# Optimization experiments

Hardware: AMD Instinct MI355X
Metric: run time of the kernel (lower is better)

Reference implementation:

```python
import jax, jax.numpy as jnp
import numpy as np
from jax import lax

NPOINT = 1024
RADIUS = 0.2
NSAMPLE = 32
BN_EPS = 1e-5


def square_distance(src, dst):
    # src: [B,N,3], dst: [B,M,3] -> [B,N,M]
    d = -2.0 * jnp.einsum('bnc,bmc->bnm', src, dst)
    d = d + jnp.sum(src * src, -1)[:, :, None]
    d = d + jnp.sum(dst * dst, -1)[:, None, :]
    return d


def farthest_point_sample(xyz, npoint):
    # Deterministic start at index 0 (torch version uses a random start).
    B, N, _ = xyz.shape
    batch = jnp.arange(B)

    def step(carry, _):
        distance, farthest = carry
        centroid = xyz[batch, farthest][:, None, :]          # [B,1,3]
        dist = jnp.sum((xyz - centroid) ** 2, -1)            # [B,N]
        distance = jnp.minimum(distance, dist)
        new_far = jnp.argmax(distance, -1).astype(jnp.int32)
        return (distance, new_far), farthest

    init = (jnp.full((B, N), 1e10, xyz.dtype), jnp.zeros((B,), jnp.int32))
    _, cents = lax.scan(step, init, None, length=npoint)     # [npoint,B]
    return cents.T                                           # [B,npoint]


def index_points(points, idx):
    # points: [B,N,C], idx: [B,...] -> [B,...,C]
    return jax.vmap(lambda p, i: p[i])(points, idx)


def query_ball_point(radius, nsample, xyz, new_xyz):
    B, N, _ = xyz.shape
    sqr = square_distance(new_xyz, xyz)                      # [B,S,N]
    gidx = jnp.where(sqr > radius * radius, N,
                     jnp.arange(N, dtype=jnp.int32)[None, None, :])
    gidx = jnp.sort(gidx, axis=-1)[:, :, :nsample]           # [B,S,nsample]
    first = gidx[:, :, :1]
    return jnp.where(gidx == N, first, gidx)


def conv_bn_relu(x, w, b, g, beta):
    # x: [B,Cin,K,S]; 1x1 conv + training-mode BN + ReLU
    y = jnp.einsum('bcks,oc->boks', x, w) + b[None, :, None, None]
    mean = jnp.mean(y, axis=(0, 2, 3), keepdims=True)
    var = jnp.var(y, axis=(0, 2, 3), keepdims=True)
    y = (y - mean) * lax.rsqrt(var + BN_EPS)
    y = y * g[None, :, None, None] + beta[None, :, None, None]
    return jax.nn.relu(y)


def setup_inputs() -> dict:
    key = jax.random.key(0)
    ks = jax.random.split(key, 8)
    B, N, D = 16, 4096, 64
    inp = {
        'xyz': jax.random.uniform(ks[0], (B, N, 3), jnp.float32),
        'points': jax.random.normal(ks[1], (B, N, D), jnp.float32),
        'w1': jax.random.normal(ks[2], (64, 67), jnp.float32) * 0.1,
        'b1': jax.random.normal(ks[3], (64,), jnp.float32) * 0.1,
        'g1': jnp.ones((64,), jnp.float32),
        'beta1': jnp.zeros((64,), jnp.float32),
        'w2': jax.random.normal(ks[4], (64, 64), jnp.float32) * 0.1,
        'b2': jax.random.normal(ks[5], (64,), jnp.float32) * 0.1,
        'g2': jnp.ones((64,), jnp.float32),
        'beta2': jnp.zeros((64,), jnp.float32),
        'w3': jax.random.normal(ks[6], (128, 64), jnp.float32) * 0.1,
        'b3': jax.random.normal(ks[7], (128,), jnp.float32) * 0.1,
        'g3': jnp.ones((128,), jnp.float32),
        'beta3': jnp.zeros((128,), jnp.float32),
    }
    return inp


def reference(xyz, points, w1, b1, g1, beta1, w2, b2, g2, beta2, w3, b3, g3, beta3):
    B, N, C = xyz.shape
    fps_idx = farthest_point_sample(xyz, NPOINT)                 # [B,S]
    new_xyz = index_points(xyz, fps_idx)                         # [B,S,3]
    idx = query_ball_point(RADIUS, NSAMPLE, xyz, new_xyz)        # [B,S,K]
    grouped_xyz = index_points(xyz, idx) - new_xyz[:, :, None, :]  # [B,S,K,3]
    grouped_points = jnp.concatenate([grouped_xyz, index_points(points, idx)], axis=-1)  # [B,S,K,3+D]
    x = jnp.transpose(grouped_points, (0, 3, 2, 1))              # [B,C,K,S]
    x = conv_bn_relu(x, w1, b1, g1, beta1)
    x = conv_bn_relu(x, w2, b2, g2, beta2)
    x = conv_bn_relu(x, w3, b3, g3, beta3)
    new_points = jnp.max(x, axis=2)                              # [B,C_out,S]
    new_points = jnp.transpose(new_points, (0, 2, 1))            # [B,S,C_out]
    return (new_xyz, new_points)
```

## Files before the change

### kernel.cpp

```cpp
#include <hip/hip_runtime.h>
#include <stdint.h>

#define NPOINT 1024
#define NSAMPLE 32
#define NB 16
#define NN 4096
#define BN_EPS 1e-5
#define NPIX (NB*NPOINT*NSAMPLE)
#define NBLK 8192

__device__ __forceinline__ float sqdist3(float dx, float dy, float dz) {
  #pragma clang fp contract(off)
  float a = dx*dx; float b = dy*dy; float c = dz*dz;
  return (a + b) + c;
}

#define FPS_T 256
#define FPS_PTS (NN/FPS_T)
#define FPS_W (FPS_T/64)

#define DPP_MAX64V(VAR, CTRL)                                                  \
  {                                                                            \
    long long kl = __double_as_longlong(VAR);                                  \
    int lo = (int)(unsigned int)kl, hi = (int)(kl >> 32);                      \
    int olo = __builtin_amdgcn_update_dpp(lo, lo, (CTRL), 0xf, 0xf, false);    \
    int ohi = __builtin_amdgcn_update_dpp(hi, hi, (CTRL), 0xf, 0xf, false);    \
    double ok = __longlong_as_double(((long long)ohi << 32) |                  \
                                     (unsigned long long)(unsigned int)olo);   \
    VAR = fmax(VAR, ok);                                                       \
  }

__global__ __launch_bounds__(256) void fps_kernel(
    const float* __restrict__ xyz, int* __restrict__ cents_g,
    float* __restrict__ out_xyz) {
  __shared__ __align__(16) float4 pos[NN];
  __shared__ __align__(16) double keybuf[2][FPS_W];
  __shared__ int cents_l[NPOINT];
  const int b = blockIdx.x;
  const int t = threadIdx.x;
  const float* base = xyz + (size_t)b * NN * 3;
  for (int i = t; i < NN; i += FPS_T) {
    pos[i] = make_float4(base[3*i+0], base[3*i+1], base[3*i+2], 0.f);
  }
  __syncthreads();
  float px[FPS_PTS], py[FPS_PTS], pz[FPS_PTS], dist[FPS_PTS];
  int lowj[FPS_PTS];
  #pragma unroll
  for (int i = 0; i < FPS_PTS; i++) {
    float4 p = pos[i*FPS_T + t];
    px[i] = p.x; py[i] = p.y; pz[i] = p.z;
    dist[i] = 1e10f;
    lowj[i] = (NN-1) - (i*FPS_T + t);
  }
  const int lane = t & 63, wid = t >> 6;
  int far = 0;
  for (int it = 0; it < NPOINT; it++) {
    if (t == 0) cents_l[it] = far;
    float4 c = pos[far];
    float nd[FPS_PTS];
    #pragma unroll
    for (int i = 0; i < FPS_PTS; i++) {
      float d = sqdist3(px[i]-c.x, py[i]-c.y, pz[i]-c.z);
      nd[i] = fminf(dist[i], d);
      dist[i] = nd[i];
    }
    double kk[FPS_PTS];
    #pragma unroll
    for (int i = 0; i < FPS_PTS; i++) {
      kk[i] = __longlong_as_double(
          ((long long)__float_as_int(nd[i]) << 32) |
          (unsigned long long)(unsigned int)lowj[i]);
    }
    double m0 = fmax(fmax(kk[0],  kk[1]),  fmax(kk[2],  kk[3]));
    double m1 = fmax(fmax(kk[4],  kk[5]),  fmax(kk[6],  kk[7]));
    double m2 = fmax(fmax(kk[8],  kk[9]),  fmax(kk[10], kk[11]));
    double m3 = fmax(fmax(kk[12], kk[13]), fmax(kk[14], kk[15]));
    double bk = fmax(fmax(m0, m1), fmax(m2, m3));
    DPP_MAX64V(bk, 0x111);
    DPP_MAX64V(bk, 0x112);
    DPP_MAX64V(bk, 0x114);
    DPP_MAX64V(bk, 0x118);
    DPP_MAX64V(bk, 0x142);
    DPP_MAX64V(bk, 0x143);
    const int p = it & 1;
    if (lane == 63) keybuf[p][wid] = bk;
    __syncthreads();
    double k = keybuf[p][lane & (FPS_W-1)];
    DPP_MAX64V(k, 0x111);
    DPP_MAX64V(k, 0x112);
    int lo32 = (int)(unsigned int)__double_as_longlong(k);
    far = (NN-1) - __builtin_amdgcn_readlane(lo32, 3);
  }
  __syncthreads();
  for (int i = t; i < NPOINT; i += FPS_T) {
    int j = cents_l[i];
    cents_g[b*NPOINT + i] = j;
    float4 p = pos[j];
    size_t o = ((size_t)b * NPOINT + i) * 3;
    out_xyz[o+0] = p.x;
    out_xyz[o+1] = p.y;
    out_xyz[o+2] = p.z;
  }
}

__global__ __launch_bounds__(256) void ballquery_kernel(
    const float* __restrict__ xyz, const int* __restrict__ cents_g,
    int* __restrict__ idx) {
  const int w = blockIdx.x * 4 + (threadIdx.x >> 6);
  const int lane = threadIdx.x & 63;
  const int b = w >> 10;
  const double RR = 0.2 * 0.2;
  const int cj = cents_g[w] & (NN-1);
  const float* cptr = xyz + ((size_t)b * NN + cj) * 3;
  const double cx = (double)cptr[0], cy = (double)cptr[1], cz = (double)cptr[2];
  const double cn = cx*cx + cy*cy + cz*cz;
  const float* base = xyz + (size_t)b * NN * 3;
  int* out = idx + (size_t)w * NSAMPLE;
  int have = 0, firstj = 0;
  for (int j0 = 0; j0 < NN; j0 += 64) {
    int j = j0 + lane;
    double x = (double)base[3*j+0];
    double y = (double)base[3*j+1];
    double z = (double)base[3*j+2];
    double pn = x*x + y*y + z*z;
    double d = -2.0*(cx*x + cy*y + cz*z) + cn + pn;
    bool pass = !(d > RR);
    unsigned long long m = __ballot(pass);
    int cnt = __popcll(m);
    if (have == 0 && cnt > 0) firstj = j0 + (__ffsll((unsigned long long)m) - 1);
    if (pass) {
      int pos = have + __popcll(m & ((1ull << lane) - 1ull));
      if (pos < NSAMPLE) out[pos] = j;
    }
    have += cnt;
    if (have >= NSAMPLE) break;
  }
  for (int k = have + lane; k < NSAMPLE; k += 64) out[k] = firstj;
}

template<int MODE, bool STOREY>
__global__ __launch_bounds__(256) void fused_pass(
    const float* __restrict__ xyz, const float* __restrict__ points,
    const int* __restrict__ cents_g, const int* __restrict__ idx,
    const float* __restrict__ w1, const float* __restrict__ b1,
    const float* __restrict__ w2, const float* __restrict__ b2,
    const float* __restrict__ w3, const float* __restrict__ b3,
    const double* __restrict__ aff1, const double* __restrict__ aff2,
    double* __restrict__ partial, float* __restrict__ pmax, float* __restrict__ pmin,
    float* __restrict__ ystore) {
  __shared__ float wbuf[67*64];
  __shared__ float xsm[67*68];
  __shared__ float bsm[64];
  __shared__ float bsm2[64];
  __shared__ float sc1m[64], sh1m[64], sc2m[64], sh2m[64];
  const int t = threadIdx.x;
  const int pb = blockIdx.x * 64;
  const int tr = t & 15, tc = t >> 4;
  double* pout = partial + (size_t)blockIdx.x * 256;

  for (int ii = t; ii < 67*64; ii += 256) {
    int oc = ii & 63, cc = ii >> 6;
    wbuf[cc*64 + oc] = w1[oc*67 + cc];
  }
  if (t < 64) {
    bsm[t] = b1[t];
    if (MODE >= 2) { sc1m[t] = (float)aff1[t]; sh1m[t] = (float)aff1[128+t]; }
    if (MODE >= 3) { sc2m[t] = (float)aff2[t]; sh2m[t] = (float)aff2[128+t]; }
  }
  {
    const int pxl = t >> 2, q = t & 3;
    const int p = pb + pxl;
    const int bs = p >> 5;
    const int b  = p >> 15;
    const int j  = idx[p] & (NN-1);
    const float4* prow = (const float4*)(points + ((size_t)b * NN + j) * 64);
    #pragma unroll
    for (int u = 0; u < 4; u++) {
      float4 v = prow[q*4 + u];
      int c0 = 3 + q*16 + u*4;
      xsm[(c0+0)*68 + pxl] = v.x;
      xsm[(c0+1)*68 + pxl] = v.y;
      xsm[(c0+2)*68 + pxl] = v.z;
      xsm[(c0+3)*68 + pxl] = v.w;
    }
    if (q == 0) {
      const float* xr = xyz + ((size_t)b * NN + j) * 3;
      const int cj = cents_g[bs] & (NN-1);
      const float* ce = xyz + ((size_t)b * NN + cj) * 3;
      xsm[0*68 + pxl] = xr[0] - ce[0];
      xsm[1*68 + pxl] = xr[1] - ce[1];
      xsm[2*68 + pxl] = xr[2] - ce[2];
    }
  }
  __syncthreads();

  float acc[4][4] = {};
  for (int cc = 0; cc < 67; cc++) {
    float4 xv = *(const float4*)&xsm[cc*68 + 4*tr];
    float4 wv = *(const float4*)&wbuf[cc*64 + 4*tc];
    float xa[4] = {xv.x, xv.y, xv.z, xv.w};
    float wa[4] = {wv.x, wv.y, wv.z, wv.w};
    #pragma unroll
    for (int i = 0; i < 4; i++)
      #pragma unroll
      for (int jj = 0; jj < 4; jj++) acc[i][jj] += xa[i]*wa[jj];
  }
  if constexpr (MODE == 1) {
    if constexpr (STOREY) {
      #pragma unroll
      for (int i = 0; i < 4; i++) {
        float4 o = make_float4(acc[i][0], acc[i][1], acc[i][2], acc[i][3]);
        *(float4*)(ystore + ((size_t)(pb + 4*tr + i))*64 + 4*tc) = o;
      }
    }
    double s1[4] = {0,0,0,0}, s2[4] = {0,0,0,0};
    #pragma unroll
    for (int jj = 0; jj < 4; jj++) {
      float bb = bsm[4*tc+jj];
      #pragma unroll
      for (int i = 0; i < 4; i++) {
        double yd = (double)(acc[i][jj] + bb);
        s1[jj] += yd; s2[jj] += yd*yd;
      }
    }
    #pragma unroll
    for (int off = 8; off > 0; off >>= 1)
      #pragma unroll
      for (int jj = 0; jj < 4; jj++) {
        s1[jj] += __shfl_down(s1[jj], off, 16);
        s2[jj] += __shfl_down(s2[jj], off, 16);
      }
    if (tr == 0)
      #pragma unroll
      for (int jj = 0; jj < 4; jj++) {
        pout[4*tc+jj]       = s1[jj];
        pout[128 + 4*tc+jj] = s2[jj];
      }
    return;
  }

  __syncthreads();
  #pragma unroll
  for (int jj = 0; jj < 4; jj++) {
    int oc = 4*tc + jj;
    float bb = bsm[oc], sc = sc1m[oc], sh = sh1m[oc];
    float r[4];
    #pragma unroll
    for (int i = 0; i < 4; i++) r[i] = fmaxf((acc[i][jj] + bb)*sc + sh, 0.f);
    *(float4*)&xsm[oc*68 + 4*tr] = make_float4(r[0], r[1], r[2], r[3]);
  }
  for (int ii = t; ii < 4096; ii += 256) {
    int oc = ii & 63, cc = ii >> 6;
    wbuf[cc*64 + oc] = w2[oc*64 + cc];
  }
  if (t < 64) bsm2[t] = b2[t];
  __syncthreads();

  float acc2[4][4] = {};
  for (int cc = 0; cc < 64; cc++) {
    float4 xv = *(const float4*)&xsm[cc*68 + 4*tr];
    float4 wv = *(const float4*)&wbuf[cc*64 + 4*tc];
    float xa[4] = {xv.x, xv.y, xv.z, xv.w};
    float wa[4] = {wv.x, wv.y, wv.z, wv.w};
    #pragma unroll
    for (int i = 0; i < 4; i++)
      #pragma unroll
      for (int jj = 0; jj < 4; jj++) acc2[i][jj] += xa[i]*wa[jj];
  }
  if constexpr (MODE == 2) {
    if constexpr (STOREY) {
      #pragma unroll
      for (int i = 0; i < 4; i++) {
        float4 o = make_float4(acc2[i][0], acc2[i][1], acc2[i][2], acc2[i][3]);
        *(float4*)(ystore + ((size_t)(pb + 4*tr + i))*64 + 4*tc) = o;
      }
    }
    double s1[4] = {0,0,0,0}, s2[4] = {0,0,0,0};
    #pragma unroll
    for (int jj = 0; jj < 4; jj++) {
      float bb = bsm2[4*tc+jj];
      #pragma unroll
      for (int i = 0; i < 4; i++) {
        double yd = (double)(acc2[i][jj] + bb);
        s1[jj] += yd; s2[jj] += yd*yd;
      }
    }
    #pragma unroll
    for (int off = 8; off > 0; off >>= 1)
      #pragma unroll
      for (int jj = 0; jj < 4; jj++) {
        s1[jj] += __shfl_down(s1[jj], off, 16);
        s2[jj] += __shfl_down(s2[jj], off, 16);
      }
    if (tr == 0)
      #pragma unroll
      for (int jj = 0; jj < 4; jj++) {
        pout[4*tc+jj]       = s1[jj];
        pout[128 + 4*tc+jj] = s2[jj];
      }
    return;
  }

  if constexpr (MODE == 3) {
    __syncthreads();
    #pragma unroll
    for (int jj = 0; jj < 4; jj++) {
      int oc = 4*tc + jj;
      float bb = bsm2[oc], sc = sc2m[oc], sh = sh2m[oc];
      float r[4];
      #pragma unroll
      for (int i = 0; i < 4; i++) r[i] = fmaxf((acc2[i][jj] + bb)*sc + sh, 0.f);
      *(float4*)&xsm[oc*68 + 4*tr] = make_float4(r[0], r[1], r[2], r[3]);
    }
    for (int h = 0; h < 2; h++) {
      for (int ii = t; ii < 4096; ii += 256) {
        int oc = ii & 63, cc = ii >> 6;
        wbuf[cc*64 + oc] = w3[(h*64 + oc)*64 + cc];
      }
      if (t < 64) bsm[t] = b3[h*64 + t];
      __syncthreads();
      float acc3[4][4] = {};
      for (int cc = 0; cc < 64; cc++) {
        float4 xv = *(const float4*)&xsm[cc*68 + 4*tr];
        float4 wv = *(const float4*)&wbuf[cc*64 + 4*tc];
        float xa[4] = {xv.x, xv.y, xv.z, xv.w};
        float wa[4] = {wv.x, wv.y, wv.z, wv.w};
        #pragma unroll
        for (int i = 0; i < 4; i++)
          #pragma unroll
          for (int jj = 0; jj < 4; jj++) acc3[i][jj] += xa[i]*wa[jj];
      }
      double s1[4] = {0,0,0,0}, s2[4] = {0,0,0,0};
      float pmx[4], pmn[4];
      #pragma unroll
      for (int jj = 0; jj < 4; jj++) { pmx[jj] = -3.4e38f; pmn[jj] = 3.4e38f; }
      #pragma unroll
      for (int jj = 0; jj < 4; jj++) {
        float bb = bsm[4*tc+jj];
        #pragma unroll
        for (int i = 0; i < 4; i++) {
          float y = acc3[i][jj] + bb;
          double yd = (double)y;
          s1[jj] += yd; s2[jj] += yd*yd;
          pmx[jj] = fmaxf(pmx[jj], y); pmn[jj] = fminf(pmn[jj], y);
        }
      }
      #pragma unroll
      for (int off = 8; off > 0; off >>= 1)
        #pragma unroll
        for (int jj = 0; jj < 4; jj++) {
          s1[jj] += __shfl_down(s1[jj], off, 16);
          s2[jj] += __shfl_down(s2[jj], off, 16);
        }
      if (tr == 0)
        #pragma unroll
        for (int jj = 0; jj < 4; jj++) {
          pout[h*64 + 4*tc+jj]       = s1[jj];
          pout[128 + h*64 + 4*tc+jj] = s2[jj];
        }
      #pragma unroll
      for (int off = 4; off > 0; off >>= 1)
        #pragma unroll
        for (int jj = 0; jj < 4; jj++) {
          pmx[jj] = fmaxf(pmx[jj], __shfl_down(pmx[jj], off, 8));
          pmn[jj] = fminf(pmn[jj], __shfl_down(pmn[jj], off, 8));
        }
      if ((tr & 7) == 0) {
        int bs = (pb >> 5) + (tr >> 3);
        size_t ob = (size_t)bs*128 + h*64 + 4*tc;
        #pragma unroll
        for (int jj = 0; jj < 4; jj++) {
          pmax[ob + jj] = pmx[jj];
          pmin[ob + jj] = pmn[jj];
        }
      }
      __syncthreads();
    }
  }
}

__global__ __launch_bounds__(256) void fused_mid(
    const float* __restrict__ y1, const float* __restrict__ b1,
    const float* __restrict__ w2, const float* __restrict__ b2,
    const double* __restrict__ aff1,
    double* __restrict__ partial, float* __restrict__ y2) {
  __shared__ float wbuf[64*64];
  __shared__ float xsm[64*68];
  __shared__ float bsm[64];
  __shared__ float bsm2[64];
  __shared__ float sc1m[64], sh1m[64];
  const int t = threadIdx.x;
  const int pb = blockIdx.x * 64;
  const int tr = t & 15, tc = t >> 4;
  double* pout = partial + (size_t)blockIdx.x * 256;

  for (int ii = t; ii < 4096; ii += 256) {
    int oc = ii & 63, cc = ii >> 6;
    wbuf[cc*64 + oc] = w2[oc*64 + cc];
  }
  if (t < 64) {
    bsm[t] = b1[t]; bsm2[t] = b2[t];
    sc1m[t] = (float)aff1[t]; sh1m[t] = (float)aff1[128+t];
  }
  __syncthreads();
  {
    const int pxl = t >> 2, q = t & 3;
    const float* yrow = y1 + ((size_t)(pb + pxl))*64;
    #pragma unroll
    for (int u = 0; u < 4; u++) {
      int c0 = 4*q + 16*u;
      float4 v = *(const float4*)(yrow + c0);
      xsm[(c0+0)*68 + pxl] = fmaxf((v.x + bsm[c0+0])*sc1m[c0+0] + sh1m[c0+0], 0.f);
      xsm[(c0+1)*68 + pxl] = fmaxf((v.y + bsm[c0+1])*sc1m[c0+1] + sh1m[c0+1], 0.f);
      xsm[(c0+2)*68 + pxl] = fmaxf((v.z + bsm[c0+2])*sc1m[c0+2] + sh1m[c0+2], 0.f);
      xsm[(c0+3)*68 + pxl] = fmaxf((v.w + bsm[c0+3])*sc1m[c0+3] + sh1m[c0+3], 0.f);
    }
  }
  __syncthreads();

  float acc2[4][4] = {};
  for (int cc = 0; cc < 64; cc++) {
    float4 xv = *(const float4*)&xsm[cc*68 + 4*tr];
    float4 wv = *(const float4*)&wbuf[cc*64 + 4*tc];
    float xa[4] = {xv.x, xv.y, xv.z, xv.w};
    float wa[4] = {wv.x, wv.y, wv.z, wv.w};
    #pragma unroll
    for (int i = 0; i < 4; i++)
      #pragma unroll
      for (int jj = 0; jj < 4; jj++) acc2[i][jj] += xa[i]*wa[jj];
  }
  #pragma unroll
  for (int i = 0; i < 4; i++) {
    float4 o = make_float4(acc2[i][0], acc2[i][1], acc2[i][2], acc2[i][3]);
    *(float4*)(y2 + ((size_t)(pb + 4*tr + i))*64 + 4*tc) = o;
  }
  double s1[4] = {0,0,0,0}, s2[4] = {0,0,0,0};
  #pragma unroll
  for (int jj = 0; jj < 4; jj++) {
    float bb = bsm2[4*tc+jj];
    #pragma unroll
    for (int i = 0; i < 4; i++) {
      double yd = (double)(acc2[i][jj] + bb);
      s1[jj] += yd; s2[jj] += yd*yd;
    }
  }
  #pragma unroll
  for (int off = 8; off > 0; off >>= 1)
    #pragma unroll
    for (int jj = 0; jj < 4; jj++) {
      s1[jj] += __shfl_down(s1[jj], off, 16);
      s2[jj] += __shfl_down(s2[jj], off, 16);
    }
  if (tr == 0)
    #pragma unroll
    for (int jj = 0; jj < 4; jj++) {
      pout[4*tc+jj]       = s1[jj];
      pout[128 + 4*tc+jj] = s2[jj];
    }
}

__global__ __launch_bounds__(256) void fused_last(
    const float* __restrict__ y2, const float* __restrict__ b2,
    const float* __restrict__ w3, const float* __restrict__ b3,
    const double* __restrict__ aff2,
    double* __restrict__ partial, float* __restrict__ pmax, float* __restrict__ pmin) {
  __shared__ float wbuf[64*64];
  __shared__ float xsm[64*68];
  __shared__ float bsm[64];
  __shared__ float bsm2[64];
  __shared__ float sc2m[64], sh2m[64];
  const int t = threadIdx.x;
  const int pb = blockIdx.x * 64;
  const int tr = t & 15, tc = t >> 4;
  double* pout = partial + (size_t)blockIdx.x * 256;

  if (t < 64) {
    bsm2[t] = b2[t];
    sc2m[t] = (float)aff2[t]; sh2m[t] = (float)aff2[128+t];
  }
  __syncthreads();
  {
    const int pxl = t >> 2, q = t & 3;
    const float* yrow = y2 + ((size_t)(pb + pxl))*64;
    #pragma unroll
    for (int u = 0; u < 4; u++) {
      int c0 = 4*q + 16*u;
      float4 v = *(const float4*)(yrow + c0);
      xsm[(c0+0)*68 + pxl] = fmaxf((v.x + bsm2[c0+0])*sc2m[c0+0] + sh2m[c0+0], 0.f);
      xsm[(c0+1)*68 + pxl] = fmaxf((v.y + bsm2[c0+1])*sc2m[c0+1] + sh2m[c0+1], 0.f);
      xsm[(c0+2)*68 + pxl] = fmaxf((v.z + bsm2[c0+2])*sc2m[c0+2] + sh2m[c0+2], 0.f);
      xsm[(c0+3)*68 + pxl] = fmaxf((v.w + bsm2[c0+3])*sc2m[c0+3] + sh2m[c0+3], 0.f);
    }
  }
  for (int h = 0; h < 2; h++) {
    for (int ii = t; ii < 4096; ii += 256) {
      int oc = ii & 63, cc = ii >> 6;
      wbuf[cc*64 + oc] = w3[(h*64 + oc)*64 + cc];
    }
    if (t < 64) bsm[t] = b3[h*64 + t];
    __syncthreads();
    float acc3[4][4] = {};
    for (int cc = 0; cc < 64; cc++) {
      float4 xv = *(const float4*)&xsm[cc*68 + 4*tr];
      float4 wv = *(const float4*)&wbuf[cc*64 + 4*tc];
      float xa[4] = {xv.x, xv.y, xv.z, xv.w};
      float wa[4] = {wv.x, wv.y, wv.z, wv.w};
      #pragma unroll
      for (int i = 0; i < 4; i++)
        #pragma unroll
        for (int jj = 0; jj < 4; jj++) acc3[i][jj] += xa[i]*wa[jj];
    }
    double s1[4] = {0,0,0,0}, s2[4] = {0,0,0,0};
    float pmx[4], pmn[4];
    #pragma unroll
    for (int jj = 0; jj < 4; jj++) { pmx[jj] = -3.4e38f; pmn[jj] = 3.4e38f; }
    #pragma unroll
    for (int jj = 0; jj < 4; jj++) {
      float bb = bsm[4*tc+jj];
      #pragma unroll
      for (int i = 0; i < 4; i++) {
        float y = acc3[i][jj] + bb;
        double yd = (double)y;
        s1[jj] += yd; s2[jj] += yd*yd;
        pmx[jj] = fmaxf(pmx[jj], y); pmn[jj] = fminf(pmn[jj], y);
      }
    }
    #pragma unroll
    for (int off = 8; off > 0; off >>= 1)
      #pragma unroll
      for (int jj = 0; jj < 4; jj++) {
        s1[jj] += __shfl_down(s1[jj], off, 16);
        s2[jj] += __shfl_down(s2[jj], off, 16);
      }
    if (tr == 0)
      #pragma unroll
      for (int jj = 0; jj < 4; jj++) {
        pout[h*64 + 4*tc+jj]       = s1[jj];
        pout[128 + h*64 + 4*tc+jj] = s2[jj];
      }
    #pragma unroll
    for (int off = 4; off > 0; off >>= 1)
      #pragma unroll
      for (int jj = 0; jj < 4; jj++) {
        pmx[jj] = fmaxf(pmx[jj], __shfl_down(pmx[jj], off, 8));
        pmn[jj] = fminf(pmn[jj], __shfl_down(pmn[jj], off, 8));
      }
    if ((tr & 7) == 0) {
      int bs = (pb >> 5) + (tr >> 3);
      size_t ob = (size_t)bs*128 + h*64 + 4*tc;
      #pragma unroll
      for (int jj = 0; jj < 4; jj++) {
        pmax[ob + jj] = pmx[jj];
        pmin[ob + jj] = pmn[jj];
      }
    }
    __syncthreads();
  }
}

__global__ __launch_bounds__(256) void reduce_stageA(
    const double* __restrict__ partial, double* __restrict__ partial2) {
  const int t = threadIdx.x;
  const int bid = blockIdx.x;
  const double* p = partial + (size_t)bid * 64 * 256 + t;
  double a0 = 0.0, a1 = 0.0, a2 = 0.0, a3 = 0.0;
  #pragma unroll 4
  for (int i = 0; i < 64; i += 4) {
    a0 += p[(size_t)(i+0)*256];
    a1 += p[(size_t)(i+1)*256];
    a2 += p[(size_t)(i+2)*256];
    a3 += p[(size_t)(i+3)*256];
  }
  partial2[(size_t)bid*256 + t] = (a0 + a1) + (a2 + a3);
}

__global__ __launch_bounds__(256) void reduce_finalize_kernel(
    const double* __restrict__ partial2,
    const float* __restrict__ g, const float* __restrict__ beta,
    double* __restrict__ aff) {
  __shared__ double sa1[4], sa2[4];
  const int c = blockIdx.x;
  const int t = threadIdx.x;
  double a1 = 0.0, a2 = 0.0;
  for (int blk = t; blk < 128; blk += 256) {
    a1 += partial2[(size_t)blk*256 + c];
    a2 += partial2[(size_t)blk*256 + 128 + c];
  }
  #pragma unroll
  for (int off = 32; off > 0; off >>= 1) {
    a1 += __shfl_down(a1, off);
    a2 += __shfl_down(a2, off);
  }
  const int lane = t & 63, wid = t >> 6;
  if (lane == 0) { sa1[wid] = a1; sa2[wid] = a2; }
  __syncthreads();
  if (t == 0) {
    double s1 = sa1[0] + sa1[1] + sa1[2] + sa1[3];
    double s2 = sa2[0] + sa2[1] + sa2[2] + sa2[3];
    const double invN = 1.0 / (double)NPIX;
    double mean = s1 * invN;
    double var  = s2 * invN - mean*mean;
    var = var > 0.0 ? var : 0.0;
    double r  = 1.0 / sqrt(var + BN_EPS);
    double sc = (double)g[c] * r;
    aff[c]       = sc;
    aff[128 + c] = (double)beta[c] - mean*sc;
  }
}

__global__ __launch_bounds__(256) void out_kernel(
    const float* __restrict__ pmax, const float* __restrict__ pmin,
    const double* __restrict__ aff3, float* __restrict__ out_np) {
  int i = blockIdx.x * 256 + threadIdx.x;
  int oc = i & 127;
  double sc = aff3[oc], sh = aff3[128+oc];
  double v = (sc >= 0.0) ? (double)pmax[i] : (double)pmin[i];
  double y = v*sc + sh;
  out_np[i] = (float)(y > 0.0 ? y : 0.0);
}

extern "C" void kernel_launch(void* const* d_in, const int* in_sizes, int n_in,
                              void* d_out, int out_size, void* d_ws, size_t ws_size,
                              hipStream_t stream) {
  const float* xyz    = (const float*)d_in[0];
  const float* points = (const float*)d_in[1];
  const float* w1  = (const float*)d_in[2];
  const float* b1  = (const float*)d_in[3];
  const float* g1  = (const float*)d_in[4];
  const float* be1 = (const float*)d_in[5];
  const float* w2  = (const float*)d_in[6];
  const float* b2  = (const float*)d_in[7];
  const float* g2  = (const float*)d_in[8];
  const float* be2 = (const float*)d_in[9];
  const float* w3  = (const float*)d_in[10];
  const float* b3  = (const float*)d_in[11];
  const float* g3  = (const float*)d_in[12];
  const float* be3 = (const float*)d_in[13];

  char* ws = (char*)d_ws;
  double* aff     = (double*)(ws + 8192);
  int*    cents   = (int*)  (ws + 16384);
  int*    idx     = (int*)  (ws + 81920);
  float*  pmax    = (float*)(ws + 2179072);
  float*  pmin    = (float*)(ws + 10567680);
  double* partial = (double*)(ws + 18956288);
  const size_t OFF_Y = 35733504;
  const size_t SZ_Y  = (size_t)NPIX * 64 * 4;
  float* ycache1 = (float*)(ws + OFF_Y);
  float* ycache2 = (float*)(ws + OFF_Y + SZ_Y);
  const bool full_path = ws_size >= OFF_Y + 2*SZ_Y;
  const bool mid_path  = ws_size >= OFF_Y + SZ_Y;
  double* p2a = (double*)pmax;
  double* p2b = (double*)idx;
  float* out_xyz = (float*)d_out;
  float* out_np  = (float*)d_out + (size_t)NB*NPOINT*3;

  fps_kernel        <<<16,   256, 0, stream>>>(xyz, cents, out_xyz);
  ballquery_kernel  <<<4096, 256, 0, stream>>>(xyz, cents, idx);
  if (full_path) {
    fused_pass<1,true>  <<<NBLK, 256, 0, stream>>>(xyz, points, cents, idx, w1,b1,w2,b2,w3,b3,
                                                   aff, aff+256, partial, pmax, pmin, ycache1);
    reduce_stageA     <<<128, 256, 0, stream>>>(partial, p2a);
    reduce_finalize_kernel<<<64, 256, 0, stream>>>(p2a, g1, be1, aff);
    fused_mid         <<<NBLK, 256, 0, stream>>>(ycache1, b1, w2, b2, aff, partial, ycache2);
    reduce_stageA     <<<128, 256, 0, stream>>>(partial, p2a);
    reduce_finalize_kernel<<<64, 256, 0, stream>>>(p2a, g2, be2, aff+256);
    fused_last        <<<NBLK, 256, 0, stream>>>(ycache2, b2, w3, b3, aff+256,
                                                 partial, pmax, pmin);
    reduce_stageA     <<<128, 256, 0, stream>>>(partial, p2b);
    reduce_finalize_kernel<<<128, 256, 0, stream>>>(p2b, g3, be3, aff+512);
  } else if (mid_path) {
    fused_pass<1,false> <<<NBLK, 256, 0, stream>>>(xyz, points, cents, idx, w1,b1,w2,b2,w3,b3,
                                                   aff, aff+256, partial, pmax, pmin, nullptr);
    reduce_stageA     <<<128, 256, 0, stream>>>(partial, p2a);
    reduce_finalize_kernel<<<64, 256, 0, stream>>>(p2a, g1, be1, aff);
    fused_pass<2,true>  <<<NBLK, 256, 0, stream>>>(xyz, points, cents, idx, w1,b1,w2,b2,w3,b3,
                                                   aff, aff+256, partial, pmax, pmin, ycache1);
    reduce_stageA     <<<128, 256, 0, stream>>>(partial, p2a);
    reduce_finalize_kernel<<<64, 256, 0, stream>>>(p2a, g2, be2, aff+256);
    fused_last        <<<NBLK, 256, 0, stream>>>(ycache1, b2, w3, b3, aff+256,
                                                 partial, pmax, pmin);
    reduce_stageA     <<<128, 256, 0, stream>>>(partial, p2b);
    reduce_finalize_kernel<<<128, 256, 0, stream>>>(p2b, g3, be3, aff+512);
  } else {
    fused_pass<1,false> <<<NBLK, 256, 0, stream>>>(xyz, points, cents, idx, w1,b1,w2,b2,w3,b3,
                                                   aff, aff+256, partial, pmax, pmin, nullptr);
    reduce_stageA     <<<128, 256, 0, stream>>>(partial, p2a);
    reduce_finalize_kernel<<<64, 256, 0, stream>>>(p2a, g1, be1, aff);
    fused_pass<2,false> <<<NBLK, 256, 0, stream>>>(xyz, points, cents, idx, w1,b1,w2,b2,w3,b3,
                                                   aff, aff+256, partial, pmax, pmin, nullptr);
    reduce_stageA     <<<128, 256, 0, stream>>>(partial, p2a);
    reduce_finalize_kernel<<<64, 256, 0, stream>>>(p2a, g2, be2, aff+256);
    fused_pass<3,false> <<<NBLK, 256, 0, stream>>>(xyz, points, cents, idx, w1,b1,w2,b2,w3,b3,
                                                   aff, aff+256, partial, pmax, pmin, nullptr);
    reduce_stageA     <<<128, 256, 0, stream>>>(partial, p2b);
    reduce_finalize_kernel<<<128, 256, 0, stream>>>(p2b, g3, be3, aff+512);
  }
  out_kernel        <<<NBLK, 256, 0, stream>>>(pmax, pmin, aff+512, out_np);
}
```

Before: 1.194 ms.

## Process two pixel tiles per block in layers 1-2 and pack FPS distance keys

Adds dedicated first-layer and mid-layer kernels that each handle two 64-pixel tiles per block, halving the block count. This amortizes the per-block weight transpose into shared memory and halves the per-block BN partial sums, so the reduction kernels get a block-count parameter. FPS now keeps packed distance/index keys in doubles and updates them with a single fmin, which removes the separate float distance array and the repack step. Fewer blocks may reduce occupancy and latency hiding.

```diff
diff --git a/kernel.cpp b/kernel.cpp
--- a/kernel.cpp
+++ b/kernel.cpp
@@ -8,6 +8,7 @@
 #define BN_EPS 1e-5
 #define NPIX (NB*NPOINT*NSAMPLE)
 #define NBLK 8192
+#define NBLK2 4096
 
 __device__ __forceinline__ float sqdist3(float dx, float dy, float dz) {
   #pragma clang fp contract(off)
@@ -43,33 +44,30 @@
     pos[i] = make_float4(base[3*i+0], base[3*i+1], base[3*i+2], 0.f);
   }
   __syncthreads();
-  float px[FPS_PTS], py[FPS_PTS], pz[FPS_PTS], dist[FPS_PTS];
+  float px[FPS_PTS], py[FPS_PTS], pz[FPS_PTS];
+  double kk[FPS_PTS];
   int lowj[FPS_PTS];
   #pragma unroll
   for (int i = 0; i < FPS_PTS; i++) {
     float4 p = pos[i*FPS_T + t];
     px[i] = p.x; py[i] = p.y; pz[i] = p.z;
-    dist[i] = 1e10f;
     lowj[i] = (NN-1) - (i*FPS_T + t);
+    kk[i] = __longlong_as_double(
+        ((long long)__float_as_int(1e10f) << 32) |
+        (unsigned long long)(unsigned int)lowj[i]);
   }
   const int lane = t & 63, wid = t >> 6;
   int far = 0;
   for (int it = 0; it < NPOINT; it++) {
     if (t == 0) cents_l[it] = far;
     float4 c = pos[far];
-    float nd[FPS_PTS];
     #pragma unroll
     for (int i = 0; i < FPS_PTS; i++) {
       float d = sqdist3(px[i]-c.x, py[i]-c.y, pz[i]-c.z);
-      nd[i] = fminf(dist[i], d);
-      dist[i] = nd[i];
-    }
-    double kk[FPS_PTS];
-    #pragma unroll
-    for (int i = 0; i < FPS_PTS; i++) {
-      kk[i] = __longlong_as_double(
-          ((long long)__float_as_int(nd[i]) << 32) |
+      double nk = __longlong_as_double(
+          ((long long)__float_as_int(d) << 32) |
           (unsigned long long)(unsigned int)lowj[i]);
+      kk[i] = fmin(kk[i], nk);
     }
     double m0 = fmax(fmax(kk[0],  kk[1]),  fmax(kk[2],  kk[3]));
     double m1 = fmax(fmax(kk[4],  kk[5]),  fmax(kk[6],  kk[7]));
@@ -138,6 +136,281 @@
   for (int k = have + lane; k < NSAMPLE; k += 64) out[k] = firstj;
 }
 
+__global__ __launch_bounds__(256) void fused_first2(
+    const float* __restrict__ xyz, const float* __restrict__ points,
+    const int* __restrict__ cents_g, const int* __restrict__ idx,
+    const float* __restrict__ w1, const float* __restrict__ b1,
+    double* __restrict__ partial, float* __restrict__ ystore) {
+  __shared__ float wbuf[67*64];
+  __shared__ float xsm[67*68];
+  __shared__ float bsm[64];
+  const int t = threadIdx.x;
+  const int pb0 = blockIdx.x * 128;
+  const int tr = t & 15, tc = t >> 4;
+  double* pout = partial + (size_t)blockIdx.x * 256;
+
+  for (int ii = t; ii < 67*64; ii += 256) {
+    int oc = ii & 63, cc = ii >> 6;
+    wbuf[cc*64 + oc] = w1[oc*67 + cc];
+  }
+  if (t < 64) bsm[t] = b1[t];
+
+  double s1[4] = {0,0,0,0}, s2[4] = {0,0,0,0};
+  for (int tile = 0; tile < 2; tile++) {
+    const int pb = pb0 + tile*64;
+    if (tile) __syncthreads();
+    {
+      const int pxl = t >> 2, q = t & 3;
+      const int p = pb + pxl;
+      const int bs = p >> 5;
+      const int b  = p >> 15;
+      const int j  = idx[p] & (NN-1);
+      const float4* prow = (const float4*)(points + ((size_t)b * NN + j) * 64);
+      #pragma unroll
+      for (int u = 0; u < 4; u++) {
+        float4 v = prow[q*4 + u];
+        int c0 = 3 + q*16 + u*4;
+        xsm[(c0+0)*68 + pxl] = v.x;
+        xsm[(c0+1)*68 + pxl] = v.y;
+        xsm[(c0+2)*68 + pxl] = v.z;
+        xsm[(c0+3)*68 + pxl] = v.w;
+      }
+      if (q == 0) {
+        const float* xr = xyz + ((size_t)b * NN + j) * 3;
+        const int cj = cents_g[bs] & (NN-1);
+        const float* ce = xyz + ((size_t)b * NN + cj) * 3;
+        xsm[0*68 + pxl] = xr[0] - ce[0];
+        xsm[1*68 + pxl] = xr[1] - ce[1];
+        xsm[2*68 + pxl] = xr[2] - ce[2];
+      }
+    }
+    __syncthreads();
+
+    float acc[4][4] = {};
+    for (int cc = 0; cc < 67; cc++) {
+      float4 xv = *(const float4*)&xsm[cc*68 + 4*tr];
+      float4 wv = *(const float4*)&wbuf[cc*64 + 4*tc];
+      float xa[4] = {xv.x, xv.y, xv.z, xv.w};
+      float wa[4] = {wv.x, wv.y, wv.z, wv.w};
+      #pragma unroll
+      for (int i = 0; i < 4; i++)
+        #pragma unroll
+        for (int jj = 0; jj < 4; jj++) acc[i][jj] += xa[i]*wa[jj];
+    }
+    #pragma unroll
+    for (int i = 0; i < 4; i++) {
+      float4 o = make_float4(acc[i][0], acc[i][1], acc[i][2], acc[i][3]);
+      *(float4*)(ystore + ((size_t)(pb + 4*tr + i))*64 + 4*tc) = o;
+    }
+    #pragma unroll
+    for (int jj = 0; jj < 4; jj++) {
+      float bb = bsm[4*tc+jj];
+      #pragma unroll
+      for (int i = 0; i < 4; i++) {
+        double yd = (double)(acc[i][jj] + bb);
+        s1[jj] += yd; s2[jj] += yd*yd;
+      }
+    }
+  }
+  #pragma unroll
+  for (int off = 8; off > 0; off >>= 1)
+    #pragma unroll
+    for (int jj = 0; jj < 4; jj++) {
+      s1[jj] += __shfl_down(s1[jj], off, 16);
+      s2[jj] += __shfl_down(s2[jj], off, 16);
+    }
+  if (tr == 0)
+    #pragma unroll
+    for (int jj = 0; jj < 4; jj++) {
+      pout[4*tc+jj]       = s1[jj];
+      pout[128 + 4*tc+jj] = s2[jj];
+    }
+}
+
+__global__ __launch_bounds__(256) void fused_mid2(
+    const float* __restrict__ y1, const float* __restrict__ b1,
+    const float* __restrict__ w2, const float* __restrict__ b2,
+    const double* __restrict__ aff1,
+    double* __restrict__ partial, float* __restrict__ y2) {
+  __shared__ float wbuf[64*64];
+  __shared__ float xsm[64*68];
+  __shared__ float bsm[64];
+  __shared__ float bsm2[64];
+  __shared__ float sc1m[64], sh1m[64];
+  const int t = threadIdx.x;
+  const int pb0 = blockIdx.x * 128;
+  const int tr = t & 15, tc = t >> 4;
+  double* pout = partial + (size_t)blockIdx.x * 256;
+
+  for (int ii = t; ii < 4096; ii += 256) {
+    int oc = ii & 63, cc = ii >> 6;
+    wbuf[cc*64 + oc] = w2[oc*64 + cc];
+  }
+  if (t < 64) {
+    bsm[t] = b1[t]; bsm2[t] = b2[t];
+    sc1m[t] = (float)aff1[t]; sh1m[t] = (float)aff1[128+t];
+  }
+
+  double s1[4] = {0,0,0,0}, s2[4] = {0,0,0,0};
+  for (int tile = 0; tile < 2; tile++) {
+    const int pb = pb0 + tile*64;
+    if (tile) __syncthreads();
+    else __syncthreads();
+    {
+      const int pxl = t >> 2, q = t & 3;
+      const float* yrow = y1 + ((size_t)(pb + pxl))*64;
+      #pragma unroll
+      for (int u = 0; u < 4; u++) {
+        int c0 = 4*q + 16*u;
+        float4 v = *(const float4*)(yrow + c0);
+        xsm[(c0+0)*68 + pxl] = fmaxf((v.x + bsm[c0+0])*sc1m[c0+0] + sh1m[c0+0], 0.f);
+        xsm[(c0+1)*68 + pxl] = fmaxf((v.y + bsm[c0+1])*sc1m[c0+1] + sh1m[c0+1], 0.f);
+        xsm[(c0+2)*68 + pxl] = fmaxf((v.z + bsm[c0+2])*sc1m[c0+2] + sh1m[c0+2], 0.f);
+        xsm[(c0+3)*68 + pxl] = fmaxf((v.w + bsm[c0+3])*sc1m[c0+3] + sh1m[c0+3], 0.f);
+      }
+    }
+    __syncthreads();
+
+    float acc2[4][4] = {};
+    for (int cc = 0; cc < 64; cc++) {
+      float4 xv = *(const float4*)&xsm[cc*68 + 4*tr];
+      float4 wv = *(const float4*)&wbuf[cc*64 + 4*tc];
+      float xa[4] = {xv.x, xv.y, xv.z, xv.w};
+      float wa[4] = {wv.x, wv.y, wv.z, wv.w};
+      #pragma unroll
+      for (int i = 0; i < 4; i++)
+        #pragma unroll
+        for (int jj = 0; jj < 4; jj++) acc2[i][jj] += xa[i]*wa[jj];
+    }
+    #pragma unroll
+    for (int i = 0; i < 4; i++) {
+      float4 o = make_float4(acc2[i][0], acc2[i][1], acc2[i][2], acc2[i][3]);
+      *(float4*)(y2 + ((size_t)(pb + 4*tr + i))*64 + 4*tc) = o;
+    }
+    #pragma unroll
+    for (int jj = 0; jj < 4; jj++) {
+      float bb = bsm2[4*tc+jj];
+      #pragma unroll
+      for (int i = 0; i < 4; i++) {
+        double yd = (double)(acc2[i][jj] + bb);
+        s1[jj] += yd; s2[jj] += yd*yd;
+      }
+    }
+  }
+  #pragma unroll
+  for (int off = 8; off > 0; off >>= 1)
+    #pragma unroll
+    for (int jj = 0; jj < 4; jj++) {
+      s1[jj] += __shfl_down(s1[jj], off, 16);
+      s2[jj] += __shfl_down(s2[jj], off, 16);
+    }
+  if (tr == 0)
+    #pragma unroll
+    for (int jj = 0; jj < 4; jj++) {
+      pout[4*tc+jj]       = s1[jj];
+      pout[128 + 4*tc+jj] = s2[jj];
+    }
+}
+
+__global__ __launch_bounds__(256) void fused_last(
+    const float* __restrict__ y2, const float* __restrict__ b2,
+    const float* __restrict__ w3, const float* __restrict__ b3,
+    const double* __restrict__ aff2,
+    double* __restrict__ partial, float* __restrict__ pmax, float* __restrict__ pmin) {
+  __shared__ float wbuf[64*64];
+  __shared__ float xsm[64*68];
+  __shared__ float bsm[64];
+  __shared__ float bsm2[64];
+  __shared__ float sc2m[64], sh2m[64];
+  const int t = threadIdx.x;
+  const int pb = blockIdx.x * 64;
+  const int tr = t & 15, tc = t >> 4;
+  double* pout = partial + (size_t)blockIdx.x * 256;
+
+  if (t < 64) {
+    bsm2[t] = b2[t];
+    sc2m[t] = (float)aff2[t]; sh2m[t] = (float)aff2[128+t];
+  }
+  __syncthreads();
+  {
+    const int pxl = t >> 2, q = t & 3;
+    const float* yrow = y2 + ((size_t)(pb + pxl))*64;
+    #pragma unroll
+    for (int u = 0; u < 4; u++) {
+      int c0 = 4*q + 16*u;
+      float4 v = *(const float4*)(yrow + c0);
+      xsm[(c0+0)*68 + pxl] = fmaxf((v.x + bsm2[c0+0])*sc2m[c0+0] + sh2m[c0+0], 0.f);
+      xsm[(c0+1)*68 + pxl] = fmaxf((v.y + bsm2[c0+1])*sc2m[c0+1] + sh2m[c0+1], 0.f);
+      xsm[(c0+2)*68 + pxl] = fmaxf((v.z + bsm2[c0+2])*sc2m[c0+2] + sh2m[c0+2], 0.f);
+      xsm[(c0+3)*68 + pxl] = fmaxf((v.w + bsm2[c0+3])*sc2m[c0+3] + sh2m[c0+3], 0.f);
+    }
+  }
+  for (int h = 0; h < 2; h++) {
+    for (int ii = t; ii < 4096; ii += 256) {
+      int oc = ii & 63, cc = ii >> 6;
+      wbuf[cc*64 + oc] = w3[(h*64 + oc)*64 + cc];
+    }
+    if (t < 64) bsm[t] = b3[h*64 + t];
+    __syncthreads();
+    float acc3[4][4] = {};
+    for (int cc = 0; cc < 64; cc++) {
+      float4 xv = *(const float4*)&xsm[cc*68 + 4*tr];
+      float4 wv = *(const float4*)&wbuf[cc*64 + 4*tc];
+      float xa[4] = {xv.x, xv.y, xv.z, xv.w};
+      float wa[4] = {wv.x, wv.y, wv.z, wv.w};
+      #pragma unroll
+      for (int i = 0; i < 4; i++)
+        #pragma unroll
+        for (int jj = 0; jj < 4; jj++) acc3[i][jj] += xa[i]*wa[jj];
+    }
+    double s1[4] = {0,0,0,0}, s2[4] = {0,0,0,0};
+    float pmx[4], pmn[4];
+    #pragma unroll
+    for (int jj = 0; jj < 4; jj++) { pmx[jj] = -3.4e38f; pmn[jj] = 3.4e38f; }
+    #pragma unroll
+    for (int jj = 0; jj < 4; jj++) {
+      float bb = bsm[4*tc+jj];
+      #pragma unroll
+      for (int i = 0; i < 4; i++) {
+        float y = acc3[i][jj] + bb;
+        double yd = (double)y;
+        s1[jj] += yd; s2[jj] += yd*yd;
+        pmx[jj] = fmaxf(pmx[jj], y); pmn[jj] = fminf(pmn[jj], y);
+      }
+    }
+    #pragma unroll
+    for (int off = 8; off > 0; off >>= 1)
+      #pragma unroll
+      for (int jj = 0; jj < 4; jj++) {
+        s1[jj] += __shfl_down(s1[jj], off, 16);
+        s2[jj] += __shfl_down(s2[jj], off, 16);
+      }
+    if (tr == 0)
+      #pragma unroll
+      for (int jj = 0; jj < 4; jj++) {
+        pout[h*64 + 4*tc+jj]       = s1[jj];
+        pout[128 + h*64 + 4*tc+jj] = s2[jj];
+      }
+    #pragma unroll
+    for (int off = 4; off > 0; off >>= 1)
+      #pragma unroll
+      for (int jj = 0; jj < 4; jj++) {
+        pmx[jj] = fmaxf(pmx[jj], __shfl_down(pmx[jj], off, 8));
+        pmn[jj] = fminf(pmn[jj], __shfl_down(pmn[jj], off, 8));
+      }
+    if ((tr & 7) == 0) {
+      int bs = (pb >> 5) + (tr >> 3);
+      size_t ob = (size_t)bs*128 + h*64 + 4*tc;
+      #pragma unroll
+      for (int jj = 0; jj < 4; jj++) {
+        pmax[ob + jj] = pmx[jj];
+        pmin[ob + jj] = pmn[jj];
+      }
+    }
+    __syncthreads();
+  }
+}
+
 template<int MODE, bool STOREY>
 __global__ __launch_bounds__(256) void fused_pass(
     const float* __restrict__ xyz, const float* __restrict__ points,
@@ -379,185 +652,6 @@
   }
 }
 
-__global__ __launch_bounds__(256) void fused_mid(
-    const float* __restrict__ y1, const float* __restrict__ b1,
-    const float* __restrict__ w2, const float* __restrict__ b2,
-    const double* __restrict__ aff1,
-    double* __restrict__ partial, float* __restrict__ y2) {
-  __shared__ float wbuf[64*64];
-  __shared__ float xsm[64*68];
-  __shared__ float bsm[64];
-  __shared__ float bsm2[64];
-  __shared__ float sc1m[64], sh1m[64];
-  const int t = threadIdx.x;
-  const int pb = blockIdx.x * 64;
-  const int tr = t & 15, tc = t >> 4;
-  double* pout = partial + (size_t)blockIdx.x * 256;
-
-  for (int ii = t; ii < 4096; ii += 256) {
-    int oc = ii & 63, cc = ii >> 6;
-    wbuf[cc*64 + oc] = w2[oc*64 + cc];
-  }
-  if (t < 64) {
-    bsm[t] = b1[t]; bsm2[t] = b2[t];
-    sc1m[t] = (float)aff1[t]; sh1m[t] = (float)aff1[128+t];
-  }
-  __syncthreads();
-  {
-    const int pxl = t >> 2, q = t & 3;
-    const float* yrow = y1 + ((size_t)(pb + pxl))*64;
-    #pragma unroll
-    for (int u = 0; u < 4; u++) {
-      int c0 = 4*q + 16*u;
-      float4 v = *(const float4*)(yrow + c0);
-      xsm[(c0+0)*68 + pxl] = fmaxf((v.x + bsm[c0+0])*sc1m[c0+0] + sh1m[c0+0], 0.f);
-      xsm[(c0+1)*68 + pxl] = fmaxf((v.y + bsm[c0+1])*sc1m[c0+1] + sh1m[c0+1], 0.f);
-      xsm[(c0+2)*68 + pxl] = fmaxf((v.z + bsm[c0+2])*sc1m[c0+2] + sh1m[c0+2], 0.f);
-      xsm[(c0+3)*68 + pxl] = fmaxf((v.w + bsm[c0+3])*sc1m[c0+3] + sh1m[c0+3], 0.f);
-    }
-  }
-  __syncthreads();
-
-  float acc2[4][4] = {};
-  for (int cc = 0; cc < 64; cc++) {
-    float4 xv = *(const float4*)&xsm[cc*68 + 4*tr];
-    float4 wv = *(const float4*)&wbuf[cc*64 + 4*tc];
-    float xa[4] = {xv.x, xv.y, xv.z, xv.w};
-    float wa[4] = {wv.x, wv.y, wv.z, wv.w};
-    #pragma unroll
-    for (int i = 0; i < 4; i++)
-      #pragma unroll
-      for (int jj = 0; jj < 4; jj++) acc2[i][jj] += xa[i]*wa[jj];
-  }
-  #pragma unroll
-  for (int i = 0; i < 4; i++) {
-    float4 o = make_float4(acc2[i][0], acc2[i][1], acc2[i][2], acc2[i][3]);
-    *(float4*)(y2 + ((size_t)(pb + 4*tr + i))*64 + 4*tc) = o;
-  }
-  double s1[4] = {0,0,0,0}, s2[4] = {0,0,0,0};
-  #pragma unroll
-  for (int jj = 0; jj < 4; jj++) {
-    float bb = bsm2[4*tc+jj];
-    #pragma unroll
-    for (int i = 0; i < 4; i++) {
-      double yd = (double)(acc2[i][jj] + bb);
-      s1[jj] += yd; s2[jj] += yd*yd;
-    }
-  }
-  #pragma unroll
-  for (int off = 8; off > 0; off >>= 1)
-    #pragma unroll
-    for (int jj = 0; jj < 4; jj++) {
-      s1[jj] += __shfl_down(s1[jj], off, 16);
-      s2[jj] += __shfl_down(s2[jj], off, 16);
-    }
-  if (tr == 0)
-    #pragma unroll
-    for (int jj = 0; jj < 4; jj++) {
-      pout[4*tc+jj]       = s1[jj];
-      pout[128 + 4*tc+jj] = s2[jj];
-    }
-}
-
-__global__ __launch_bounds__(256) void fused_last(
-    const float* __restrict__ y2, const float* __restrict__ b2,
-    const float* __restrict__ w3, const float* __restrict__ b3,
-    const double* __restrict__ aff2,
-    double* __restrict__ partial, float* __restrict__ pmax, float* __restrict__ pmin) {
-  __shared__ float wbuf[64*64];
-  __shared__ float xsm[64*68];
-  __shared__ float bsm[64];
-  __shared__ float bsm2[64];
-  __shared__ float sc2m[64], sh2m[64];
-  const int t = threadIdx.x;
-  const int pb = blockIdx.x * 64;
-  const int tr = t & 15, tc = t >> 4;
-  double* pout = partial + (size_t)blockIdx.x * 256;
-
-  if (t < 64) {
-    bsm2[t] = b2[t];
-    sc2m[t] = (float)aff2[t]; sh2m[t] = (float)aff2[128+t];
-  }
-  __syncthreads();
-  {
-    const int pxl = t >> 2, q = t & 3;
-    const float* yrow = y2 + ((size_t)(pb + pxl))*64;
-    #pragma unroll
-    for (int u = 0; u < 4; u++) {
-      int c0 = 4*q + 16*u;
-      float4 v = *(const float4*)(yrow + c0);
-      xsm[(c0+0)*68 + pxl] = fmaxf((v.x + bsm2[c0+0])*sc2m[c0+0] + sh2m[c0+0], 0.f);
-      xsm[(c0+1)*68 + pxl] = fmaxf((v.y + bsm2[c0+1])*sc2m[c0+1] + sh2m[c0+1], 0.f);
-      xsm[(c0+2)*68 + pxl] = fmaxf((v.z + bsm2[c0+2])*sc2m[c0+2] + sh2m[c0+2], 0.f);
-      xsm[(c0+3)*68 + pxl] = fmaxf((v.w + bsm2[c0+3])*sc2m[c0+3] + sh2m[c0+3], 0.f);
-    }
-  }
-  for (int h = 0; h < 2; h++) {
-    for (int ii = t; ii < 4096; ii += 256) {
-      int oc = ii & 63, cc = ii >> 6;
-      wbuf[cc*64 + oc] = w3[(h*64 + oc)*64 + cc];
-    }
-    if (t < 64) bsm[t] = b3[h*64 + t];
-    __syncthreads();
-    float acc3[4][4] = {};
-    for (int cc = 0; cc < 64; cc++) {
-      float4 xv = *(const float4*)&xsm[cc*68 + 4*tr];
-      float4 wv = *(const float4*)&wbuf[cc*64 + 4*tc];
-      float xa[4] = {xv.x, xv.y, xv.z, xv.w};
-      float wa[4] = {wv.x, wv.y, wv.z, wv.w};
-      #pragma unroll
-      for (int i = 0; i < 4; i++)
-        #pragma unroll
-        for (int jj = 0; jj < 4; jj++) acc3[i][jj] += xa[i]*wa[jj];
-    }
-    double s1[4] = {0,0,0,0}, s2[4] = {0,0,0,0};
-    float pmx[4], pmn[4];
-    #pragma unroll
-    for (int jj = 0; jj < 4; jj++) { pmx[jj] = -3.4e38f; pmn[jj] = 3.4e38f; }
-    #pragma unroll
-    for (int jj = 0; jj < 4; jj++) {
-      float bb = bsm[4*tc+jj];
-      #pragma unroll
-      for (int i = 0; i < 4; i++) {
-        float y = acc3[i][jj] + bb;
-        double yd = (double)y;
-        s1[jj] += yd; s2[jj] += yd*yd;
-        pmx[jj] = fmaxf(pmx[jj], y); pmn[jj] = fminf(pmn[jj], y);
-      }
-    }
-    #pragma unroll
-    for (int off = 8; off > 0; off >>= 1)
-      #pragma unroll
-      for (int jj = 0; jj < 4; jj++) {
-        s1[jj] += __shfl_down(s1[jj], off, 16);
-        s2[jj] += __shfl_down(s2[jj], off, 16);
-      }
-    if (tr == 0)
-      #pragma unroll
-      for (int jj = 0; jj < 4; jj++) {
-        pout[h*64 + 4*tc+jj]       = s1[jj];
-        pout[128 + h*64 + 4*tc+jj] = s2[jj];
-      }
-    #pragma unroll
-    for (int off = 4; off > 0; off >>= 1)
-      #pragma unroll
-      for (int jj = 0; jj < 4; jj++) {
-        pmx[jj] = fmaxf(pmx[jj], __shfl_down(pmx[jj], off, 8));
-        pmn[jj] = fminf(pmn[jj], __shfl_down(pmn[jj], off, 8));
-      }
-    if ((tr & 7) == 0) {
-      int bs = (pb >> 5) + (tr >> 3);
-      size_t ob = (size_t)bs*128 + h*64 + 4*tc;
-      #pragma unroll
-      for (int jj = 0; jj < 4; jj++) {
-        pmax[ob + jj] = pmx[jj];
-        pmin[ob + jj] = pmn[jj];
-      }
-    }
-    __syncthreads();
-  }
-}
-
 __global__ __launch_bounds__(256) void reduce_stageA(
     const double* __restrict__ partial, double* __restrict__ partial2) {
   const int t = threadIdx.x;
@@ -577,12 +671,12 @@
 __global__ __launch_bounds__(256) void reduce_finalize_kernel(
     const double* __restrict__ partial2,
     const float* __restrict__ g, const float* __restrict__ beta,
-    double* __restrict__ aff) {
+    double* __restrict__ aff, int nb2) {
   __shared__ double sa1[4], sa2[4];
   const int c = blockIdx.x;
   const int t = threadIdx.x;
   double a1 = 0.0, a2 = 0.0;
-  for (int blk = t; blk < 128; blk += 256) {
+  for (int blk = t; blk < nb2; blk += 256) {
     a1 += partial2[(size_t)blk*256 + c];
     a2 += partial2[(size_t)blk*256 + 128 + c];
   }
@@ -658,43 +752,54 @@
   fps_kernel        <<<16,   256, 0, stream>>>(xyz, cents, out_xyz);
   ballquery_kernel  <<<4096, 256, 0, stream>>>(xyz, cents, idx);
   if (full_path) {
-    fused_pass<1,true>  <<<NBLK, 256, 0, stream>>>(xyz, points, cents, idx, w1,b1,w2,b2,w3,b3,
-                                                   aff, aff+256, partial, pmax, pmin, ycache1);
-    reduce_stageA     <<<128, 256, 0, stream>>>(partial, p2a);
-    reduce_finalize_kernel<<<64, 256, 0, stream>>>(p2a, g1, be1, aff);
-    fused_mid         <<<NBLK, 256, 0, stream>>>(ycache1, b1, w2, b2, aff, partial, ycache2);
-    reduce_stageA     <<<128, 256, 0, stream>>>(partial, p2a);
-    reduce_finalize_kernel<<<64, 256, 0, stream>>>(p2a, g2, be2, aff+256);
+    fused_first2      <<<NBLK2, 256, 0, stream>>>(xyz, points, cents, idx, w1, b1,
+                                                  partial, ycache1);
+    reduce_stageA     <<<64,  256, 0, stream>>>(partial, p2a);
+    reduce_finalize_kernel<<<64, 256, 0, stream>>>(p2a, g1, be1, aff, 64);
+    fused_mid2        <<<NBLK2, 256, 0, stream>>>(ycache1, b1, w2, b2, aff, partial,
+                                                  ycache2);
+    reduce_stageA     <<<64,  256, 0, stream>>>(partial, p2a);
+    reduce_finalize_kernel<<<64, 256, 0, stream>>>(p2a, g2, be2, aff+256, 64);
     fused_last        <<<NBLK, 256, 0, stream>>>(ycache2, b2, w3, b3, aff+256,
                                                  partial, pmax, pmin);
     reduce_stageA     <<<128, 256, 0, stream>>>(partial, p2b);
-    reduce_finalize_kernel<<<128, 256, 0, stream>>>(p2b, g3, be3, aff+512);
+    reduce_finalize_kernel<<<128, 256, 0, stream>>>(p2b, g3, be3, aff+512, 128);
   } else if (mid_path) {
-    fused_pass<1,false> <<<NBLK, 256, 0, stream>>>(xyz, points, cents, idx, w1,b1,w2,b2,w3,b3,
-                                                   aff, aff+256, partial, pmax, pmin, nullptr);
+    fused_pass<1,false> <<<NBLK, 256, 0, stream>>>(xyz, points, cents, idx,
+                                                   w1,b1,w2,b2,w3,b3,
+                                                   aff, aff+256, partial, pmax, pmin,
+                                                   nullptr);
     reduce_stageA     <<<128, 256, 0, stream>>>(partial, p2a);
-    reduce_finalize_kernel<<<64, 256, 0, stream>>>(p2a, g1, be1, aff);
-    fused_pass<2,true>  <<<NBLK, 256, 0, stream>>>(xyz, points, cents, idx, w1,b1,w2,b2,w3,b3,
-                                                   aff, aff+256, partial, pmax, pmin, ycache1);
+    reduce_finalize_kernel<<<64, 256, 0, stream>>>(p2a, g1, be1, aff, 128);
+    fused_pass<2,true>  <<<NBLK, 256, 0, stream>>>(xyz, points, cents, idx,
+                                                   w1,b1,w2,b2,w3,b3,
+                                                   aff, aff+256, partial, pmax, pmin,
+                                                   ycache1);
     reduce_stageA     <<<128, 256, 0, stream>>>(partial, p2a);
-    reduce_finalize_kernel<<<64, 256, 0, stream>>>(p2a, g2, be2, aff+256);
+    reduce_finalize_kernel<<<64, 256, 0, stream>>>(p2a, g2, be2, aff+256, 128);
     fused_last        <<<NBLK, 256, 0, stream>>>(ycache1, b2, w3, b3, aff+256,
                                                  partial, pmax, pmin);
     reduce_stageA     <<<128, 256, 0, stream>>>(partial, p2b);
-    reduce_finalize_kernel<<<128, 256, 0, stream>>>(p2b, g3, be3, aff+512);
+    reduce_finalize_kernel<<<128, 256, 0, stream>>>(p2b, g3, be3, aff+512, 128);
   } else {
-    fused_pass<1,false> <<<NBLK, 256, 0, stream>>>(xyz, points, cents, idx, w1,b1,w2,b2,w3,b3,
-                                                   aff, aff+256, partial, pmax, pmin, nullptr);
+    fused_pass<1,false> <<<NBLK, 256, 0, stream>>>(xyz, points, cents, idx,
+                                                   w1,b1,w2,b2,w3,b3,
+                                                   aff, aff+256, partial, pmax, pmin,
+                                                   nullptr);
     reduce_stageA     <<<128, 256, 0, stream>>>(partial, p2a);
-    reduce_finalize_kernel<<<64, 256, 0, stream>>>(p2a, g1, be1, aff);
-    fused_pass<2,false> <<<NBLK, 256, 0, stream>>>(xyz, points, cents, idx, w1,b1,w2,b2,w3,b3,
-                                                   aff, aff+256, partial, pmax, pmin, nullptr);
+    reduce_finalize_kernel<<<64, 256, 0, stream>>>(p2a, g1, be1, aff, 128);
+    fused_pass<2,false> <<<NBLK, 256, 0, stream>>>(xyz, points, cents, idx,
+                                                   w1,b1,w2,b2,w3,b3,
+                                                   aff, aff+256, partial, pmax, pmin,
+                                                   nullptr);
     reduce_stageA     <<<128, 256, 0, stream>>>(partial, p2a);
-    reduce_finalize_kernel<<<64, 256, 0, stream>>>(p2a, g2, be2, aff+256);
-    fused_pass<3,false> <<<NBLK, 256, 0, stream>>>(xyz, points, cents, idx, w1,b1,w2,b2,w3,b3,
-                                                   aff, aff+256, partial, pmax, pmin, nullptr);
+    reduce_finalize_kernel<<<64, 256, 0, stream>>>(p2a, g2, be2, aff+256, 128);
+    fused_pass<3,false> <<<NBLK, 256, 0, stream>>>(xyz, points, cents, idx,
+                                                   w1,b1,w2,b2,w3,b3,
+                                                   aff, aff+256, partial, pmax, pmin,
+                                                   nullptr);
     reduce_stageA     <<<128, 256, 0, stream>>>(partial, p2b);
-    reduce_finalize_kernel<<<128, 256, 0, stream>>>(p2b, g3, be3, aff+512);
+    reduce_finalize_kernel<<<128, 256, 0, stream>>>(p2b, g3, be3, aff+512, 128);
   }
   out_kernel        <<<NBLK, 256, 0, stream>>>(pmax, pmin, aff+512, out_np);
 }
```

After: 1.169 ms. 2.1% less time.
